# Performance work log

Measured on AMD Instinct MI355X. Metric: run time of the kernel, lower is better.

## Reference

```python
import jax, jax.numpy as jnp
import numpy as np

TEMPERATURE = 0.1
EPS = 1e-8  # matches torch F.cosine_similarity norm clamp

N, D = 4096, 256

def setup_inputs() -> dict:
    key = jax.random.key(0)
    k1, k2 = jax.random.split(key)
    z_i = jax.random.normal(k1, (N, D), dtype=jnp.float32)
    z_j = jax.random.normal(k2, (N, D), dtype=jnp.float32)
    return {"z_i": z_i, "z_j": z_j}

def reference(z_i, z_j):
    n = z_i.shape[0]
    z = jnp.concatenate([z_i, z_j], axis=0)              # [2N, D]
    # cosine similarity via normalized Gram matrix (faithful to F.cosine_similarity)
    norms = jnp.maximum(jnp.linalg.norm(z, axis=-1, keepdims=True), EPS)
    zn = z / norms                                        # [2N, D]
    sim = (zn @ zn.T) / TEMPERATURE                       # [2N, 2N]
    # mask self-similarity on the diagonal
    diag = jnp.eye(2 * n, dtype=bool)
    sim = jnp.where(diag, -jnp.inf, sim)
    # labels: positive of i is i+N (and vice versa)
    labels = jnp.concatenate([jnp.arange(n, 2 * n), jnp.arange(0, n)])
    logp = jax.nn.log_softmax(sim, axis=-1)               # [2N, 2N]
    nll = -jnp.take_along_axis(logp, labels[:, None], axis=-1)[:, 0]
    return jnp.mean(nll)
```

## Files before the change

### kernel.cpp

```cpp
#include <hip/hip_runtime.h>
#include <hip/hip_bf16.h>

#define NHALF 4096
#define TWO_N 8192
#define DDIM 256
#define INV_T 10.0f
#define SCALE 14.426950408889634f
#define KBSTRIDE ((size_t)TWO_N * 64)

typedef __bf16 v8bf __attribute__((ext_vector_type(8)));
typedef float f32x4 __attribute__((ext_vector_type(4)));

#if __has_builtin(__builtin_amdgcn_exp2f)
#define EXP2F(x) __builtin_amdgcn_exp2f(x)
#else
#define EXP2F(x) exp2f(x)
#endif

static __device__ __forceinline__ unsigned int f2bf(float x) {
    __hip_bfloat16 h = __float2bfloat16(x);
    return (unsigned int)*(unsigned short*)&h;
}

__global__ __launch_bounds__(256) void ntx_norm_kernel(
    const float* __restrict__ zi, const float* __restrict__ zj,
    char* __restrict__ znB, float* __restrict__ rowacc,
    float* __restrict__ out) {
    const int w = threadIdx.x >> 6;
    const int lane = threadIdx.x & 63;
    const int r = blockIdx.x * 4 + w;
    const float* src = (r < NHALF) ? (zi + (size_t)r * DDIM)
                                   : (zj + (size_t)(r - NHALF) * DDIM);
    float4 v = ((const float4*)src)[lane];
    float ss = v.x * v.x + v.y * v.y + v.z * v.z + v.w * v.w;
#pragma unroll
    for (int m = 1; m < 64; m <<= 1) ss += __shfl_xor(ss, m);
    float rinv = 1.0f / fmaxf(sqrtf(ss), 1e-8f);
    uint2 pk;
    pk.x = f2bf(v.x * rinv) | (f2bf(v.y * rinv) << 16);
    pk.y = f2bf(v.z * rinv) | (f2bf(v.w * rinv) << 16);
    char* dst = znB + (size_t)(lane >> 3) * KBSTRIDE + (size_t)r * 64 +
                ((lane >> 1) & 3) * 16 + (lane & 1) * 8;
    *(uint2*)dst = pk;
    if (blockIdx.x < 32) rowacc[blockIdx.x * 256 + threadIdx.x] = 0.0f;
    if (blockIdx.x == 0 && threadIdx.x == 0) out[0] = 0.0f;
}

__global__ __launch_bounds__(256, 2) void ntx_gram_kernel(
    const char* __restrict__ znB,
    float* __restrict__ rowacc,
    float* __restrict__ spos) {
    const int tid = threadIdx.x;
    const int w = tid >> 6, lane = tid & 63;
    const int task = blockIdx.x * 4 + w;
    const int rt = task >> 4, g = task & 15;
    const int rbase = rt * 64;
    const int lrow = lane & 15, lk = lane >> 4;
    const int nt = (g == 15 && rt < 64) ? 5 : 4;

    f32x4 af[4][8];
#pragma unroll
    for (int rf = 0; rf < 4; ++rf) {
        const char* ab =
            znB + (size_t)(rbase + rf * 16 + lrow) * 64 + lk * 16;
#pragma unroll
        for (int kb = 0; kb < 8; ++kb)
            af[rf][kb] = *(const f32x4*)(ab + kb * KBSTRIDE);
    }
#pragma unroll
    for (int rf = 0; rf < 4; ++rf)
#pragma unroll
        for (int kb = 0; kb < 8; ++kb)
            asm volatile("" : "+v"(af[rf][kb]));

    bool odg[4];
#pragma unroll
    for (int j = 0; j < 4; ++j) odg[j] = (lrow == lk * 4 + j);

    float rowsum[4][4];
#pragma unroll
    for (int rf = 0; rf < 4; ++rf)
#pragma unroll
        for (int j = 0; j < 4; ++j) rowsum[rf][j] = 0.0f;

#define LOADB(bf, cf)                                                         \
    do {                                                                      \
        _Pragma("unroll")                                                     \
        for (int kb = 0; kb < 8; ++kb)                                        \
            bf[kb] = *(const f32x4*)(zcb + (cf) * 1024 + kb * KBSTRIDE);      \
    } while (0)

#define COMPUTE_EPI(bf, cf)                                                   \
    do {                                                                      \
        f32x4 acc[4];                                                         \
        _Pragma("unroll")                                                     \
        for (int rf = 0; rf < 4; ++rf) acc[rf] = (f32x4){0.f, 0.f, 0.f, 0.f}; \
        _Pragma("unroll")                                                     \
        for (int kb = 0; kb < 8; ++kb) {                                      \
            _Pragma("unroll")                                                 \
            for (int rf = 0; rf < 4; ++rf)                                    \
                acc[rf] = __builtin_amdgcn_mfma_f32_16x16x32_bf16(            \
                    __builtin_bit_cast(v8bf, af[rf][kb]),                     \
                    __builtin_bit_cast(v8bf, bf[kb]), acc[rf], 0, 0, 0);      \
        }                                                                     \
        float ce = 0.0f;                                                      \
        _Pragma("unroll")                                                     \
        for (int rf = 0; rf < 4; ++rf) {                                      \
            const bool dfrag = (rf == (cf));                                  \
            _Pragma("unroll")                                                 \
            for (int j = 0; j < 4; ++j) {                                     \
                const float sv = acc[rf][j];                                  \
                const bool od = dfrag && odg[j];                              \
                if (posb && od) {                                             \
                    const int u = rf * 16 + lk * 4 + j;                       \
                    spos[rbase + u] = sv * INV_T;                             \
                    spos[cb + u] = sv * INV_T;                                \
                }                                                             \
                float e = EXP2F(sv * SCALE);                                  \
                e = (self && od) ? 0.0f : e;                                  \
                rowsum[rf][j] += e;                                           \
                ce += e;                                                      \
            }                                                                 \
        }                                                                     \
        if (!self) {                                                          \
            ce += __shfl_xor(ce, 16);                                         \
            ce += __shfl_xor(ce, 32);                                         \
            if (lane < 16)                                                    \
                atomicAdd(&rowacc[cb + (cf) * 16 + lrow], ce);                \
        }                                                                     \
    } while (0)

#pragma unroll 1
    for (int s = 0; s < nt; ++s) {
        const int d = (s < 4) ? (g * 4 + s) : 64;
        const int ct = (rt - d + 128) & 127;
        const int cb = ct * 64;
        const bool self = (d == 0);
        const bool posb = (d == 64);
        const char* zcb = znB + (size_t)(cb + lrow) * 64 + lk * 16;
        f32x4 bfA[8], bfB[8];
        LOADB(bfA, 0);
        LOADB(bfB, 1);
        COMPUTE_EPI(bfA, 0);
        LOADB(bfA, 2);
        COMPUTE_EPI(bfB, 1);
        LOADB(bfB, 3);
        COMPUTE_EPI(bfA, 2);
        COMPUTE_EPI(bfB, 3);
    }
#undef LOADB
#undef COMPUTE_EPI

#pragma unroll
    for (int rf = 0; rf < 4; ++rf) {
#pragma unroll
        for (int j = 0; j < 4; ++j) {
            float v = rowsum[rf][j];
            v += __shfl_xor(v, 1);
            v += __shfl_xor(v, 2);
            v += __shfl_xor(v, 4);
            v += __shfl_xor(v, 8);
            if (lrow == 0)
                atomicAdd(&rowacc[rbase + rf * 16 + lk * 4 + j], v);
        }
    }
}

__global__ __launch_bounds__(256) void ntx_final_kernel(
    const float* __restrict__ rowacc, const float* __restrict__ spos,
    float* __restrict__ out) {
    const int tid = threadIdx.x;
    const int r = blockIdx.x * 256 + tid;
    float nll = logf(rowacc[r]) - spos[r];
    __shared__ float red[256];
    red[tid] = nll;
    __syncthreads();
    for (int s = 128; s > 0; s >>= 1) {
        if (tid < s) red[tid] += red[tid + s];
        __syncthreads();
    }
    if (tid == 0) atomicAdd(out, red[0] * (1.0f / (float)TWO_N));
}

extern "C" void kernel_launch(void* const* d_in, const int* in_sizes, int n_in,
                              void* d_out, int out_size, void* d_ws, size_t ws_size,
                              hipStream_t stream) {
    const float* zi = (const float*)d_in[0];
    const float* zj = (const float*)d_in[1];
    char* ws = (char*)d_ws;
    char* znB = ws;
    size_t off = (size_t)TWO_N * DDIM * 2;
    float* spos = (float*)(ws + off);
    off += (size_t)TWO_N * 4;
    float* rowacc = (float*)(ws + off);
    float* out = (float*)d_out;

    ntx_norm_kernel<<<TWO_N / 4, 256, 0, stream>>>(zi, zj, znB, rowacc, out);
    ntx_gram_kernel<<<512, 256, 0, stream>>>(znB, rowacc, spos);
    ntx_final_kernel<<<TWO_N / 256, 256, 0, stream>>>(rowacc, spos, out);
}
```

Before: 44.73 us.

## Split gram kernel into one-wave blocks with separate positive-tile blocks

The gram kernel now runs one 64-thread wave per block across 2064 blocks instead of four-wave blocks. The 64 positive-pair diagonal tiles move to 16 dedicated blocks, so each regular wave handles exactly four tiles and the uneven fifth tile no longer stalls some waves. It also uses a single B buffer with MFMA issue raised via s_setprio, and specializes the self/posb flags at compile time. This is meant to balance load and improve scheduling, at the cost of more blocks, and the 16 positive blocks each run four tiles serially with an A reload per tile.

```diff
diff --git a/kernel.cpp b/kernel.cpp
--- a/kernel.cpp
+++ b/kernel.cpp
@@ -46,55 +46,58 @@
     if (blockIdx.x == 0 && threadIdx.x == 0) out[0] = 0.0f;
 }
 
-__global__ __launch_bounds__(256, 2) void ntx_gram_kernel(
+__global__ __launch_bounds__(64, 2) void ntx_gram_kernel(
     const char* __restrict__ znB,
     float* __restrict__ rowacc,
     float* __restrict__ spos) {
-    const int tid = threadIdx.x;
-    const int w = tid >> 6, lane = tid & 63;
-    const int task = blockIdx.x * 4 + w;
-    const int rt = task >> 4, g = task & 15;
-    const int rbase = rt * 64;
+    const int lane = threadIdx.x;
     const int lrow = lane & 15, lk = lane >> 4;
-    const int nt = (g == 15 && rt < 64) ? 5 : 4;
-
-    f32x4 af[4][8];
-#pragma unroll
-    for (int rf = 0; rf < 4; ++rf) {
-        const char* ab =
-            znB + (size_t)(rbase + rf * 16 + lrow) * 64 + lk * 16;
-#pragma unroll
-        for (int kb = 0; kb < 8; ++kb)
-            af[rf][kb] = *(const f32x4*)(ab + kb * KBSTRIDE);
-    }
-#pragma unroll
-    for (int rf = 0; rf < 4; ++rf)
-#pragma unroll
-        for (int kb = 0; kb < 8; ++kb)
-            asm volatile("" : "+v"(af[rf][kb]));
 
     bool odg[4];
 #pragma unroll
     for (int j = 0; j < 4; ++j) odg[j] = (lrow == lk * 4 + j);
 
+    f32x4 af[4][8], bf[8], acc[4];
     float rowsum[4][4];
-#pragma unroll
-    for (int rf = 0; rf < 4; ++rf)
-#pragma unroll
-        for (int j = 0; j < 4; ++j) rowsum[rf][j] = 0.0f;
-
-#define LOADB(bf, cf)                                                         \
+    int rbase;
+
+#define LOAD_AF()                                                             \
+    do {                                                                      \
+        _Pragma("unroll")                                                     \
+        for (int rf = 0; rf < 4; ++rf) {                                      \
+            const char* ab =                                                  \
+                znB + (size_t)(rbase + rf * 16 + lrow) * 64 + lk * 16;        \
+            _Pragma("unroll")                                                 \
+            for (int kb = 0; kb < 8; ++kb)                                    \
+                af[rf][kb] = *(const f32x4*)(ab + kb * KBSTRIDE);             \
+        }                                                                     \
+        _Pragma("unroll")                                                     \
+        for (int rf = 0; rf < 4; ++rf)                                        \
+            _Pragma("unroll")                                                 \
+            for (int kb = 0; kb < 8; ++kb)                                    \
+                asm volatile("" : "+v"(af[rf][kb]));                 \
+    } while (0)
+
+#define ZERO_RS()                                                             \
+    do {                                                                      \
+        _Pragma("unroll")                                                     \
+        for (int rf = 0; rf < 4; ++rf)                                        \
+            _Pragma("unroll")                                                 \
+            for (int j = 0; j < 4; ++j) rowsum[rf][j] = 0.0f;                 \
+    } while (0)
+
+#define LOADB(cf)                                                             \
     do {                                                                      \
         _Pragma("unroll")                                                     \
         for (int kb = 0; kb < 8; ++kb)                                        \
             bf[kb] = *(const f32x4*)(zcb + (cf) * 1024 + kb * KBSTRIDE);      \
     } while (0)
 
-#define COMPUTE_EPI(bf, cf)                                                   \
-    do {                                                                      \
-        f32x4 acc[4];                                                         \
+#define MFMAB()                                                               \
+    do {                                                                      \
         _Pragma("unroll")                                                     \
         for (int rf = 0; rf < 4; ++rf) acc[rf] = (f32x4){0.f, 0.f, 0.f, 0.f}; \
+        __builtin_amdgcn_s_setprio(1);                                        \
         _Pragma("unroll")                                                     \
         for (int kb = 0; kb < 8; ++kb) {                                      \
             _Pragma("unroll")                                                 \
@@ -103,67 +106,100 @@
                     __builtin_bit_cast(v8bf, af[rf][kb]),                     \
                     __builtin_bit_cast(v8bf, bf[kb]), acc[rf], 0, 0, 0);      \
         }                                                                     \
-        float ce = 0.0f;                                                      \
+        __builtin_amdgcn_s_setprio(0);                                        \
+    } while (0)
+
+#define EPI(cf, SELF, POSB, cbase)                                            \
+    do {                                                                      \
+        float fce[4];                                                         \
         _Pragma("unroll")                                                     \
         for (int rf = 0; rf < 4; ++rf) {                                      \
             const bool dfrag = (rf == (cf));                                  \
+            float p = 0.0f;                                                   \
             _Pragma("unroll")                                                 \
             for (int j = 0; j < 4; ++j) {                                     \
                 const float sv = acc[rf][j];                                  \
                 const bool od = dfrag && odg[j];                              \
-                if (posb && od) {                                             \
+                if ((POSB) && od) {                                           \
                     const int u = rf * 16 + lk * 4 + j;                       \
                     spos[rbase + u] = sv * INV_T;                             \
-                    spos[cb + u] = sv * INV_T;                                \
+                    spos[(cbase) + u] = sv * INV_T;                           \
                 }                                                             \
                 float e = EXP2F(sv * SCALE);                                  \
-                e = (self && od) ? 0.0f : e;                                  \
+                e = ((SELF) && od) ? 0.0f : e;                                \
                 rowsum[rf][j] += e;                                           \
-                ce += e;                                                      \
+                p += e;                                                       \
             }                                                                 \
-        }                                                                     \
-        if (!self) {                                                          \
+            fce[rf] = p;                                                      \
+        }                                                                     \
+        if (!(SELF)) {                                                        \
+            float ce = (fce[0] + fce[1]) + (fce[2] + fce[3]);                 \
             ce += __shfl_xor(ce, 16);                                         \
             ce += __shfl_xor(ce, 32);                                         \
             if (lane < 16)                                                    \
-                atomicAdd(&rowacc[cb + (cf) * 16 + lrow], ce);                \
-        }                                                                     \
-    } while (0)
-
+                atomicAdd(&rowacc[(cbase) + (cf) * 16 + lrow], ce);           \
+        }                                                                     \
+    } while (0)
+
+#define DO_TILE(dd, SELF, POSB)                                               \
+    do {                                                                      \
+        const int ct = (((rbase >> 6) - (dd)) + 128) & 127;                   \
+        const int cb = ct * 64;                                               \
+        const char* zcb = znB + (size_t)(cb + lrow) * 64 + lk * 16;           \
+        LOADB(0);                                                             \
+        MFMAB(); LOADB(1); EPI(0, SELF, POSB, cb);                            \
+        MFMAB(); LOADB(2); EPI(1, SELF, POSB, cb);                            \
+        MFMAB(); LOADB(3); EPI(2, SELF, POSB, cb);                            \
+        MFMAB();           EPI(3, SELF, POSB, cb);                            \
+    } while (0)
+
+#define FLUSH_RS()                                                            \
+    do {                                                                      \
+        _Pragma("unroll")                                                     \
+        for (int rf = 0; rf < 4; ++rf) {                                      \
+            _Pragma("unroll")                                                 \
+            for (int j = 0; j < 4; ++j) {                                     \
+                float v = rowsum[rf][j];                                      \
+                v += __shfl_xor(v, 1);                                        \
+                v += __shfl_xor(v, 2);                                        \
+                v += __shfl_xor(v, 4);                                        \
+                v += __shfl_xor(v, 8);                                        \
+                if (lrow == 0)                                                \
+                    atomicAdd(&rowacc[rbase + rf * 16 + lk * 4 + j], v);      \
+            }                                                                 \
+        }                                                                     \
+    } while (0)
+
+    if (blockIdx.x < 16) {
 #pragma unroll 1
-    for (int s = 0; s < nt; ++s) {
-        const int d = (s < 4) ? (g * 4 + s) : 64;
-        const int ct = (rt - d + 128) & 127;
-        const int cb = ct * 64;
-        const bool self = (d == 0);
-        const bool posb = (d == 64);
-        const char* zcb = znB + (size_t)(cb + lrow) * 64 + lk * 16;
-        f32x4 bfA[8], bfB[8];
-        LOADB(bfA, 0);
-        LOADB(bfB, 1);
-        COMPUTE_EPI(bfA, 0);
-        LOADB(bfA, 2);
-        COMPUTE_EPI(bfB, 1);
-        LOADB(bfB, 3);
-        COMPUTE_EPI(bfA, 2);
-        COMPUTE_EPI(bfB, 3);
+        for (int s = 0; s < 4; ++s) {
+            rbase = (blockIdx.x * 4 + s) * 64;
+            LOAD_AF();
+            ZERO_RS();
+            DO_TILE(64, false, true);
+            FLUSH_RS();
+        }
+    } else {
+        const int t = blockIdx.x - 16;
+        const int rt = t >> 4, g = t & 15;
+        rbase = rt * 64;
+        LOAD_AF();
+        ZERO_RS();
+#pragma unroll 1
+        for (int s = 0; s < 4; ++s) {
+            const int d = g * 4 + s;
+            const bool self = (d == 0);
+            DO_TILE(d, self, false);
+        }
+        FLUSH_RS();
     }
+#undef LOAD_AF
+#undef ZERO_RS
 #undef LOADB
-#undef COMPUTE_EPI
-
-#pragma unroll
-    for (int rf = 0; rf < 4; ++rf) {
-#pragma unroll
-        for (int j = 0; j < 4; ++j) {
-            float v = rowsum[rf][j];
-            v += __shfl_xor(v, 1);
-            v += __shfl_xor(v, 2);
-            v += __shfl_xor(v, 4);
-            v += __shfl_xor(v, 8);
-            if (lrow == 0)
-                atomicAdd(&rowacc[rbase + rf * 16 + lk * 4 + j], v);
-        }
-    }
+#undef MFMAB
+#undef EPI
+#undef DO_TILE
+#undef FLUSH_RS
 }
 
 __global__ __launch_bounds__(256) void ntx_final_kernel(
@@ -196,6 +232,6 @@
     float* out = (float*)d_out;
 
     ntx_norm_kernel<<<TWO_N / 4, 256, 0, stream>>>(zi, zj, znB, rowacc, out);
-    ntx_gram_kernel<<<512, 256, 0, stream>>>(znB, rowacc, spos);
+    ntx_gram_kernel<<<2064, 64, 0, stream>>>(znB, rowacc, spos);
     ntx_final_kernel<<<TWO_N / 256, 256, 0, stream>>>(rowacc, spos, out);
 }
```

Result: slower. 50.81 us (+13.6%).
